# Performance work log

Hardware: AMD Instinct MI355X
Metric: run time of the kernel (lower is better)

Reference implementation:

```python
import jax, jax.numpy as jnp
import numpy as np

N_NODES = 100000
N_EDGES = 640000
F_IN = 128
HID = 128
N_CLS = 40


def _glorot(key, fan_in, fan_out):
    lim = float(np.sqrt(6.0 / (fan_in + fan_out)))
    return jax.random.uniform(key, (fan_in, fan_out), jnp.float32, -lim, lim)


def setup_inputs() -> dict:
    key = jax.random.key(0)
    ks = jax.random.split(key, 10)
    x = jax.random.normal(ks[0], (N_NODES, F_IN), jnp.float32)
    edge_index = jax.random.randint(ks[1], (2, N_EDGES), 0, N_NODES, jnp.int64 if jax.config.jax_enable_x64 else jnp.int32)
    W1 = _glorot(ks[2], F_IN, HID)
    W2 = _glorot(ks[3], HID, HID)
    W3 = _glorot(ks[4], HID, HID)
    W4 = _glorot(ks[5], HID, N_CLS)
    b1 = jnp.zeros((HID,), jnp.float32)
    b2 = jnp.zeros((HID,), jnp.float32)
    b3 = jnp.zeros((HID,), jnp.float32)
    b4 = jnp.zeros((N_CLS,), jnp.float32)
    return {"x": x, "edge_index": edge_index,
            "W1": W1, "b1": b1, "W2": W2, "b2": b2,
            "W3": W3, "b3": b3, "W4": W4, "b4": b4}


def _prep_edges(edge_index, n):
    # add self-loops, compute symmetric normalization deg^{-1/2}[src]*deg^{-1/2}[dst]
    loop = jnp.arange(n, dtype=edge_index.dtype)
    src = jnp.concatenate([edge_index[0], loop])
    dst = jnp.concatenate([edge_index[1], loop])
    deg = jax.ops.segment_sum(jnp.ones_like(dst, jnp.float32), dst, num_segments=n)
    dinv = jnp.where(deg > 0, jax.lax.rsqrt(deg), 0.0)
    norm = dinv[src] * dinv[dst]  # [E + n]
    return src, dst, norm


def _gcn_conv(x, W, b, src, dst, norm, n):
    h = x @ W                      # dense linear transform [n, out]
    msg = h[src] * norm[:, None]   # gather + scale over edges
    out = jax.ops.segment_sum(msg, dst, num_segments=n)  # scatter-add
    return out + b


def reference(x, edge_index, W1, b1, W2, b2, W3, b3, W4, b4):
    n = x.shape[0]
    src, dst, norm = _prep_edges(edge_index, n)
    h = jax.nn.relu(_gcn_conv(x, W1, b1, src, dst, norm, n))
    h = jax.nn.relu(_gcn_conv(h, W2, b2, src, dst, norm, n))
    h = jax.nn.relu(_gcn_conv(h, W3, b3, src, dst, norm, n))
    h = _gcn_conv(h, W4, b4, src, dst, norm, n)
    return jax.nn.log_softmax(h, axis=1)
```

## Files before the change

### kernel.cpp

```cpp
#include <hip/hip_runtime.h>
#include <math.h>

#define N_NODES 100000
#define N_EDGES 640000

typedef __bf16 bf16x8 __attribute__((ext_vector_type(8)));
typedef float f32x4 __attribute__((ext_vector_type(4)));

__device__ __forceinline__ unsigned short f2b(float x) {
  unsigned int u = __float_as_uint(x);
  u = (u + 0x7FFFu + ((u >> 16) & 1u)) >> 16;
  return (unsigned short)u;
}
__device__ __forceinline__ float blo(unsigned int v) { return __uint_as_float(v << 16); }
__device__ __forceinline__ float bhi(unsigned int v) { return __uint_as_float(v & 0xFFFF0000u); }


__global__ __launch_bounds__(256) void k_count(const int* __restrict__ dst, int* __restrict__ deg, int e) {
  int i = blockIdx.x * 256 + threadIdx.x;
  if (i < e) atomicAdd(&deg[dst[i]], 1);
}

__global__ __launch_bounds__(256) void k_alloc(const int* __restrict__ deg, int* __restrict__ row_ptr,
                                               int* __restrict__ fillpos, int* __restrict__ col,
                                               float* __restrict__ dinv, int* __restrict__ counter, int n) {
  __shared__ int sdata[256];
  __shared__ int sbase;
  int tid = threadIdx.x;
  int i = blockIdx.x * 256 + tid;
  int d = (i < n) ? deg[i] : 0;
  sdata[tid] = d;
  __syncthreads();
  for (int off = 1; off < 256; off <<= 1) {
    int v = (tid >= off) ? sdata[tid - off] : 0;
    __syncthreads();
    sdata[tid] += v;
    __syncthreads();
  }
  if (tid == 255) sbase = atomicAdd(counter, sdata[255]);
  __syncthreads();
  int base = sbase;
  if (i < n) {
    int rp = base + sdata[tid] - d;
    row_ptr[i] = rp;
    fillpos[i] = rp + 1;
    col[rp] = i;
    dinv[i] = rsqrtf((float)d);
  }
}

__global__ __launch_bounds__(256) void k_fill(const int* __restrict__ src, const int* __restrict__ dst,
                                              int* __restrict__ fillpos, int* __restrict__ col, int e) {
  int i = blockIdx.x * 256 + threadIdx.x;
  if (i < e) {
    int d = dst[i];
    int p = atomicAdd(&fillpos[d], 1);
    col[p] = src[i];
  }
}


__global__ __launch_bounds__(256) void k_prep0(const float* __restrict__ W1, const float* __restrict__ W2,
                                               const float* __restrict__ W3, const float* __restrict__ W4,
                                               unsigned short* __restrict__ Wt, unsigned short* __restrict__ Wt4,
                                               unsigned short* __restrict__ Ha, unsigned short* __restrict__ Hc,
                                               unsigned short* __restrict__ H4,
                                               int* __restrict__ deg, int* __restrict__ counter, int n) {
  int b = blockIdx.x;
  int tid = threadIdx.x;
  if (b < 391) {
    int i = b * 256 + tid;
    if (i < n) deg[i] = 1;
    if (i == 0) *counter = 0;
  } else if (b < 583) {
    int bb = b - 391;
    const float* W = (bb < 64) ? W1 : (bb < 128) ? W2 : W3;
    unsigned short* D = Wt + ((bb < 64) ? 0 : (bb < 128) ? 16384 : 32768);
    int idx = (bb & 63) * 256 + tid;
    int k = idx >> 7, nn = idx & 127;
    D[nn * 128 + k] = f2b(W[idx]);
  } else if (b < 607) {
    int idx = (b - 583) * 256 + tid;
    int nn = idx >> 7, k = idx & 127;
    Wt4[nn * 128 + k] = (nn < 40) ? f2b(W4[(size_t)k * 40 + nn]) : (unsigned short)0;
  } else if (b == 607) {
    if (tid < 128) Ha[(size_t)n * 128 + tid] = 0;
    else Hc[(size_t)n * 128 + (tid - 128)] = 0;
  } else {
    if (tid < 48) H4[(size_t)n * 40 + tid] = 0;
  }
}

#define SXP 136


__global__ __launch_bounds__(256) void k_gemm1(const float* __restrict__ X,
                                               const unsigned short* __restrict__ Wt,
                                               const float* __restrict__ dinv,
                                               unsigned short* __restrict__ H, int n) {
  __shared__ unsigned short sW[128 * SXP];
  int tid = threadIdx.x;
  int row0 = blockIdx.x * 64;
  {
    const uint4* Wt4 = (const uint4*)Wt;
#pragma unroll
    for (int i = 0; i < 8; ++i) {
      int f = tid + i * 256;
      *(uint4*)&sW[(f >> 4) * SXP + (f & 15) * 8] = Wt4[f];
    }
  }
  int wave = tid >> 6, lane = tid & 63;
  int m = lane & 15, q = lane >> 4;
  int grow = row0 + wave * 16 + m;
  if (grow >= n) grow = n - 1;
  const float4* X4 = (const float4*)X;
  uint4 a4[4];
#pragma unroll
  for (int kc = 0; kc < 4; ++kc) {
    float4 f0 = X4[(size_t)grow * 32 + kc * 8 + q * 2];
    float4 f1 = X4[(size_t)grow * 32 + kc * 8 + q * 2 + 1];
    a4[kc].x = (unsigned int)f2b(f0.x) | ((unsigned int)f2b(f0.y) << 16);
    a4[kc].y = (unsigned int)f2b(f0.z) | ((unsigned int)f2b(f0.w) << 16);
    a4[kc].z = (unsigned int)f2b(f1.x) | ((unsigned int)f2b(f1.y) << 16);
    a4[kc].w = (unsigned int)f2b(f1.z) | ((unsigned int)f2b(f1.w) << 16);
  }
  __syncthreads();
  f32x4 acc[8];
#pragma unroll
  for (int ct = 0; ct < 8; ++ct) acc[ct] = (f32x4){0.f, 0.f, 0.f, 0.f};
#pragma unroll
  for (int kc = 0; kc < 4; ++kc) {
    bf16x8 a = *(bf16x8*)&a4[kc];
#pragma unroll
    for (int ct = 0; ct < 8; ++ct) {
      bf16x8 b = *(const bf16x8*)&sW[(ct * 16 + m) * SXP + kc * 32 + q * 8];
      acc[ct] = __builtin_amdgcn_mfma_f32_16x16x32_bf16(a, b, acc[ct], 0, 0, 0);
    }
  }
#pragma unroll
  for (int r = 0; r < 4; ++r) {
    int row = row0 + wave * 16 + q * 4 + r;
    if (row < n) {
      float di = dinv[row];
#pragma unroll
      for (int ct = 0; ct < 8; ++ct)
        H[(size_t)row * 128 + ct * 16 + m] = f2b(acc[ct][r] * di);
    }
  }
}


template <int NCT>
__global__ __launch_bounds__(256) void k_fag(const unsigned short* __restrict__ Hin,
                                             const int* __restrict__ col,
                                             const int* __restrict__ row_ptr,
                                             const int* __restrict__ deg,
                                             const float* __restrict__ dinv,
                                             const float* __restrict__ bias,
                                             const unsigned short* __restrict__ Wt,
                                             unsigned short* __restrict__ Hout, int n) {
  __shared__ unsigned short sW[NCT * 16 * SXP];
  __shared__ unsigned short sX[64 * SXP];
  int tid = threadIdx.x;
  int row0 = blockIdx.x * 64;
  {
    const uint4* W4 = (const uint4*)Wt;
#pragma unroll
    for (int i = 0; i < NCT; ++i) {
      int f = tid + i * 256;
      *(uint4*)&sW[(f >> 4) * SXP + (f & 15) * 8] = W4[f];
    }
  }
  int ql = tid & 15;
  int qbase = tid & 48;
  const uint4* Hg = (const uint4*)Hin;
  float4 b0 = ((const float4*)bias)[ql * 2];
  float4 b1 = ((const float4*)bias)[ql * 2 + 1];
  int starts[4], cnts[4], mycs[4];
#pragma unroll
  for (int it = 0; it < 4; ++it) {
    int node = row0 + (tid >> 4) + (it << 4);
    int nc = (node < n) ? node : 0;
    starts[it] = row_ptr[nc];
    cnts[it] = deg[nc];
  }
#pragma unroll
  for (int it = 0; it < 4; ++it) {
    int c0 = (cnts[it] < 15) ? cnts[it] : 15;
    mycs[it] = (ql < c0) ? col[starts[it] + ql] : n;
  }
#pragma unroll 1
  for (int it = 0; it < 4; ++it) {
    int node = row0 + (tid >> 4) + (it << 4);
    if (node >= n) break;
    int cnt = cnts[it];
    int cnt0 = (cnt < 15) ? cnt : 15;
    int myc = mycs[it];
    float s0 = 0.f, s1 = 0.f, s2 = 0.f, s3 = 0.f, s4 = 0.f, s5 = 0.f, s6 = 0.f, s7 = 0.f;
    for (int base = 0; base < cnt0; base += 8) {
      uint4 v[8];
#pragma unroll
      for (int jj = 0; jj < 8; ++jj) {
        int idx = base + jj;
        idx = (idx > 15) ? 15 : idx;
        int c = __shfl(myc, qbase + idx, 64);
        v[jj] = Hg[(size_t)c * 16 + ql];
      }
#pragma unroll
      for (int jj = 0; jj < 8; ++jj) {
        s0 += blo(v[jj].x); s1 += bhi(v[jj].x);
        s2 += blo(v[jj].y); s3 += bhi(v[jj].y);
        s4 += blo(v[jj].z); s5 += bhi(v[jj].z);
        s6 += blo(v[jj].w); s7 += bhi(v[jj].w);
      }
    }
    for (int j = 15; j < cnt; ++j) {
      int c = col[starts[it] + j];
      uint4 v = Hg[(size_t)c * 16 + ql];
      s0 += blo(v.x); s1 += bhi(v.x);
      s2 += blo(v.y); s3 += bhi(v.y);
      s4 += blo(v.z); s5 += bhi(v.z);
      s6 += blo(v.w); s7 += bhi(v.w);
    }
    float di = dinv[node];
    float o0 = fmaf(s0, di, b0.x), o1 = fmaf(s1, di, b0.y);
    float o2 = fmaf(s2, di, b0.z), o3 = fmaf(s3, di, b0.w);
    float o4 = fmaf(s4, di, b1.x), o5 = fmaf(s5, di, b1.y);
    float o6 = fmaf(s6, di, b1.z), o7 = fmaf(s7, di, b1.w);
    o0 = o0 > 0.f ? o0 : 0.f; o1 = o1 > 0.f ? o1 : 0.f;
    o2 = o2 > 0.f ? o2 : 0.f; o3 = o3 > 0.f ? o3 : 0.f;
    o4 = o4 > 0.f ? o4 : 0.f; o5 = o5 > 0.f ? o5 : 0.f;
    o6 = o6 > 0.f ? o6 : 0.f; o7 = o7 > 0.f ? o7 : 0.f;
    uint4 w;
    w.x = (unsigned int)f2b(o0) | ((unsigned int)f2b(o1) << 16);
    w.y = (unsigned int)f2b(o2) | ((unsigned int)f2b(o3) << 16);
    w.z = (unsigned int)f2b(o4) | ((unsigned int)f2b(o5) << 16);
    w.w = (unsigned int)f2b(o6) | ((unsigned int)f2b(o7) << 16);
    *(uint4*)&sX[(node - row0) * SXP + ql * 8] = w;
  }
  __syncthreads();
  int wave = tid >> 6, lane = tid & 63;
  int m = lane & 15, q = lane >> 4;
  int grow = row0 + wave * 16 + m;
  if (grow >= n) grow = n - 1;
  int lrow = grow - row0;
  uint4 a4[4];
#pragma unroll
  for (int kc = 0; kc < 4; ++kc) a4[kc] = *(const uint4*)&sX[lrow * SXP + kc * 32 + q * 8];
  f32x4 acc[NCT];
#pragma unroll
  for (int ct = 0; ct < NCT; ++ct) acc[ct] = (f32x4){0.f, 0.f, 0.f, 0.f};
#pragma unroll
  for (int kc = 0; kc < 4; ++kc) {
    bf16x8 a = *(bf16x8*)&a4[kc];
#pragma unroll
    for (int ct = 0; ct < NCT; ++ct) {
      bf16x8 b = *(const bf16x8*)&sW[(ct * 16 + m) * SXP + kc * 32 + q * 8];
      acc[ct] = __builtin_amdgcn_mfma_f32_16x16x32_bf16(a, b, acc[ct], 0, 0, 0);
    }
  }
#pragma unroll
  for (int r = 0; r < 4; ++r) {
    int row = row0 + wave * 16 + q * 4 + r;
    if (row < n) {
      float di = dinv[row];
      if constexpr (NCT == 8) {
#pragma unroll
        for (int ct = 0; ct < 8; ++ct)
          Hout[(size_t)row * 128 + ct * 16 + m] = f2b(acc[ct][r] * di);
      } else {
#pragma unroll
        for (int ct = 0; ct < NCT; ++ct) {
          int c = ct * 16 + m;
          if (c < 40) Hout[(size_t)row * 40 + c] = f2b(acc[ct][r] * di);
        }
      }
    }
  }
}


__global__ __launch_bounds__(256) void k_agg40_lsm(const unsigned short* __restrict__ H, const int* __restrict__ col,
                                                   const int* __restrict__ row_ptr, const int* __restrict__ deg,
                                                   const float* __restrict__ dinv, const float* __restrict__ bias,
                                                   float* __restrict__ out, int n) {
  int node = blockIdx.x * 4 + (threadIdx.x >> 6);
  int lane = threadIdx.x & 63;
  if (node >= n) return;
  const unsigned int* H1 = (const unsigned int*)H;
  int start = row_ptr[node];
  int cnt = deg[node];
  int cnt0 = (cnt < 63) ? cnt : 63;
  int myc = (lane < cnt0) ? col[start + lane] : n;
  int slice = (lane >= 20) + (lane >= 40);
  int pr = lane - slice * 20;
  pr = (pr > 19) ? 19 : pr;
  int rounds = (cnt0 + 2) / 3;
  float ax = 0.f, ay = 0.f;
  for (int rb = 0; rb < rounds; rb += 4) {
    unsigned int v[4];
#pragma unroll
    for (int j = 0; j < 4; ++j) {
      int idx = (rb + j) * 3 + slice;
      idx = (idx > 63) ? 63 : idx;
      int c = __shfl(myc, idx, 64);
      v[j] = H1[(size_t)c * 20 + pr];
    }
#pragma unroll
    for (int j = 0; j < 4; ++j) { ax += blo(v[j]); ay += bhi(v[j]); }
  }
  if (lane < 20) {
    for (int j = 63; j < cnt; ++j) {
      int c = col[start + j];
      unsigned int v = H1[(size_t)c * 20 + pr];
      ax += blo(v);
      ay += bhi(v);
    }
  }
  float ax1 = __shfl(ax, lane + 20, 64), ay1 = __shfl(ay, lane + 20, 64);
  float ax2 = __shfl(ax, lane + 40, 64), ay2 = __shfl(ay, lane + 40, 64);
  float di = dinv[node];
  float2 b2 = ((const float2*)bias)[pr];
  float c0 = fmaf(ax + ax1 + ax2, di, b2.x);
  float c1 = fmaf(ay + ay1 + ay2, di, b2.y);
  float v = (lane < 20) ? fmaxf(c0, c1) : -INFINITY;
#pragma unroll
  for (int off = 32; off > 0; off >>= 1) v = fmaxf(v, __shfl_xor(v, off, 64));
  float e = (lane < 20) ? (__expf(c0 - v) + __expf(c1 - v)) : 0.f;
#pragma unroll
  for (int off = 32; off > 0; off >>= 1) e += __shfl_xor(e, off, 64);
  if (lane < 20) {
    float ls = v + __logf(e);
    ((float2*)out)[(size_t)node * 20 + lane] = make_float2(c0 - ls, c1 - ls);
  }
}


extern "C" void kernel_launch(void* const* d_in, const int* in_sizes, int n_in,
                              void* d_out, int out_size, void* d_ws, size_t ws_size,
                              hipStream_t stream) {
  const float* x  = (const float*)d_in[0];
  const int* edge = (const int*)d_in[1];
  const float* W1 = (const float*)d_in[2];
  const float* b1 = (const float*)d_in[3];
  const float* W2 = (const float*)d_in[4];
  const float* b2 = (const float*)d_in[5];
  const float* W3 = (const float*)d_in[6];
  const float* b3 = (const float*)d_in[7];
  const float* W4 = (const float*)d_in[8];
  const float* b4 = (const float*)d_in[9];
  float* out = (float*)d_out;

  const int n = N_NODES, E = N_EDGES;
  const int* srcp = edge;
  const int* dstp = edge + E;

  char* ws = (char*)d_ws;
  size_t off = 0;
  auto alloc = [&](size_t bytes) -> void* {
    void* p = ws + off;
    off = (off + bytes + 255) & ~(size_t)255;
    return p;
  };
  int*   deg     = (int*)alloc((size_t)n * 4);
  int*   row_ptr = (int*)alloc((size_t)n * 4);
  int*   fillpos = (int*)alloc((size_t)n * 4);
  float* dinv    = (float*)alloc((size_t)n * 4);
  int*   counter = (int*)alloc(256);
  int*   colx    = (int*)alloc((size_t)(E + n) * 4);
  unsigned short* Ha  = (unsigned short*)alloc((size_t)(n + 1) * 128 * 2);
  unsigned short* Hc  = (unsigned short*)alloc((size_t)(n + 1) * 128 * 2);
  unsigned short* H4  = (unsigned short*)alloc(((size_t)(n + 1) * 40 + 16) * 2);
  unsigned short* Wt  = (unsigned short*)alloc((size_t)3 * 128 * 128 * 2);
  unsigned short* Wt4 = (unsigned short*)alloc((size_t)48 * 128 * 2);
  (void)ws_size; (void)in_sizes; (void)n_in; (void)out_size;

  k_prep0<<<609, 256, 0, stream>>>(W1, W2, W3, W4, Wt, Wt4, Ha, Hc, H4, deg, counter, n);
  k_count<<<(E + 255) / 256, 256, 0, stream>>>(dstp, deg, E);
  k_alloc<<<(n + 255) / 256, 256, 0, stream>>>(deg, row_ptr, fillpos, colx, dinv, counter, n);
  k_fill <<<(E + 255) / 256, 256, 0, stream>>>(srcp, dstp, fillpos, colx, E);

  const int gg = (n + 63) / 64, ga = (n + 3) / 4;
  k_gemm1<<<gg, 256, 0, stream>>>(x, Wt, dinv, Ha, n);
  k_fag<8><<<gg, 256, 0, stream>>>(Ha, colx, row_ptr, deg, dinv, b1, Wt + 16384, Hc, n);
  k_fag<8><<<gg, 256, 0, stream>>>(Hc, colx, row_ptr, deg, dinv, b2, Wt + 32768, Ha, n);
  k_fag<3><<<gg, 256, 0, stream>>>(Ha, colx, row_ptr, deg, dinv, b3, Wt4, H4, n);
  k_agg40_lsm<<<ga, 256, 0, stream>>>(H4, colx, row_ptr, deg, dinv, b4, out, n);
}
```

Measured before the change: 331.8 us.

## Pre-swizzle weights into MFMA fragment order and load B directly from global

The weight matrices are now written at prep time in MFMA B-fragment order, so each lane reads its bf16x8 operand with one coalesced 16-byte global load. This removes the per-block staging of weights into LDS and the barrier in the GEMM and fused aggregate-GEMM kernels, cutting LDS use (which may raise occupancy) and per-block setup. In exchange, every wave re-reads the weights from L2/L1 instead of sharing one LDS copy, which relies on cache hits for the small weight matrices.

```diff
diff --git a/kernel.cpp b/kernel.cpp
--- a/kernel.cpp
+++ b/kernel.cpp
@@ -14,6 +14,12 @@
 }
 __device__ __forceinline__ float blo(unsigned int v) { return __uint_as_float(v << 16); }
 __device__ __forceinline__ float bhi(unsigned int v) { return __uint_as_float(v & 0xFFFF0000u); }
+
+__device__ __forceinline__ int fragidx(int nn, int k) {
+  int ct = nn >> 4, m = nn & 15;
+  int kc = k >> 5, q = (k >> 3) & 3, e = k & 7;
+  return (((ct * 4 + kc) * 4 + q) * 16 + m) * 8 + e;
+}
 
 
 __global__ __launch_bounds__(256) void k_count(const int* __restrict__ dst, int* __restrict__ deg, int e) {
@@ -78,11 +84,11 @@
     unsigned short* D = Wt + ((bb < 64) ? 0 : (bb < 128) ? 16384 : 32768);
     int idx = (bb & 63) * 256 + tid;
     int k = idx >> 7, nn = idx & 127;
-    D[nn * 128 + k] = f2b(W[idx]);
+    D[fragidx(nn, k)] = f2b(W[idx]);
   } else if (b < 607) {
     int idx = (b - 583) * 256 + tid;
     int nn = idx >> 7, k = idx & 127;
-    Wt4[nn * 128 + k] = (nn < 40) ? f2b(W4[(size_t)k * 40 + nn]) : (unsigned short)0;
+    Wt4[fragidx(nn, k)] = (nn < 40) ? f2b(W4[(size_t)k * 40 + nn]) : (unsigned short)0;
   } else if (b == 607) {
     if (tid < 128) Ha[(size_t)n * 128 + tid] = 0;
     else Hc[(size_t)n * 128 + (tid - 128)] = 0;
@@ -98,17 +104,8 @@
                                                const unsigned short* __restrict__ Wt,
                                                const float* __restrict__ dinv,
                                                unsigned short* __restrict__ H, int n) {
-  __shared__ unsigned short sW[128 * SXP];
   int tid = threadIdx.x;
   int row0 = blockIdx.x * 64;
-  {
-    const uint4* Wt4 = (const uint4*)Wt;
-#pragma unroll
-    for (int i = 0; i < 8; ++i) {
-      int f = tid + i * 256;
-      *(uint4*)&sW[(f >> 4) * SXP + (f & 15) * 8] = Wt4[f];
-    }
-  }
   int wave = tid >> 6, lane = tid & 63;
   int m = lane & 15, q = lane >> 4;
   int grow = row0 + wave * 16 + m;
@@ -124,7 +121,7 @@
     a4[kc].z = (unsigned int)f2b(f1.x) | ((unsigned int)f2b(f1.y) << 16);
     a4[kc].w = (unsigned int)f2b(f1.z) | ((unsigned int)f2b(f1.w) << 16);
   }
-  __syncthreads();
+  const bf16x8* Wf = (const bf16x8*)Wt;
   f32x4 acc[8];
 #pragma unroll
   for (int ct = 0; ct < 8; ++ct) acc[ct] = (f32x4){0.f, 0.f, 0.f, 0.f};
@@ -133,7 +130,7 @@
     bf16x8 a = *(bf16x8*)&a4[kc];
 #pragma unroll
     for (int ct = 0; ct < 8; ++ct) {
-      bf16x8 b = *(const bf16x8*)&sW[(ct * 16 + m) * SXP + kc * 32 + q * 8];
+      bf16x8 b = Wf[(ct * 4 + kc) * 64 + lane];
       acc[ct] = __builtin_amdgcn_mfma_f32_16x16x32_bf16(a, b, acc[ct], 0, 0, 0);
     }
   }
@@ -159,18 +156,9 @@
                                              const float* __restrict__ bias,
                                              const unsigned short* __restrict__ Wt,
                                              unsigned short* __restrict__ Hout, int n) {
-  __shared__ unsigned short sW[NCT * 16 * SXP];
   __shared__ unsigned short sX[64 * SXP];
   int tid = threadIdx.x;
   int row0 = blockIdx.x * 64;
-  {
-    const uint4* W4 = (const uint4*)Wt;
-#pragma unroll
-    for (int i = 0; i < NCT; ++i) {
-      int f = tid + i * 256;
-      *(uint4*)&sW[(f >> 4) * SXP + (f & 15) * 8] = W4[f];
-    }
-  }
   int ql = tid & 15;
   int qbase = tid & 48;
   const uint4* Hg = (const uint4*)Hin;
@@ -247,6 +235,7 @@
   uint4 a4[4];
 #pragma unroll
   for (int kc = 0; kc < 4; ++kc) a4[kc] = *(const uint4*)&sX[lrow * SXP + kc * 32 + q * 8];
+  const bf16x8* Wf = (const bf16x8*)Wt;
   f32x4 acc[NCT];
 #pragma unroll
   for (int ct = 0; ct < NCT; ++ct) acc[ct] = (f32x4){0.f, 0.f, 0.f, 0.f};
@@ -255,7 +244,7 @@
     bf16x8 a = *(bf16x8*)&a4[kc];
 #pragma unroll
     for (int ct = 0; ct < NCT; ++ct) {
-      bf16x8 b = *(const bf16x8*)&sW[(ct * 16 + m) * SXP + kc * 32 + q * 8];
+      bf16x8 b = Wf[(ct * 4 + kc) * 64 + lane];
       acc[ct] = __builtin_amdgcn_mfma_f32_16x16x32_bf16(a, b, acc[ct], 0, 0, 0);
     }
   }
```

Result: slower. 340.6 us (+2.6%).

## Pad last-layer features to 64 and aggregate with 8 lanes per node using 16-byte loads

Applied to the files above, without the earlier changes.

The last-layer hidden buffer is padded from 40 to 64 bf16 columns so each row is 128 bytes, and the final GEMM writes all 4 column tiles without masking. The aggregation plus log-softmax kernel now gives each node 8 lanes, each gathering a 16-byte chunk per neighbor, instead of 64 lanes doing 4-byte loads split three ways. This cuts instruction count and improves coalescing of the gather. In exchange it adds padding bandwidth and wastes 3 of 8 lanes, and the extra MFMA tile adds a little compute.

```diff
diff --git a/kernel.cpp b/kernel.cpp
--- a/kernel.cpp
+++ b/kernel.cpp
@@ -79,15 +79,15 @@
     int idx = (bb & 63) * 256 + tid;
     int k = idx >> 7, nn = idx & 127;
     D[nn * 128 + k] = f2b(W[idx]);
-  } else if (b < 607) {
+  } else if (b < 615) {
     int idx = (b - 583) * 256 + tid;
     int nn = idx >> 7, k = idx & 127;
     Wt4[nn * 128 + k] = (nn < 40) ? f2b(W4[(size_t)k * 40 + nn]) : (unsigned short)0;
-  } else if (b == 607) {
+  } else if (b == 615) {
     if (tid < 128) Ha[(size_t)n * 128 + tid] = 0;
     else Hc[(size_t)n * 128 + (tid - 128)] = 0;
   } else {
-    if (tid < 48) H4[(size_t)n * 40 + tid] = 0;
+    if (tid < 64) H4[(size_t)n * 64 + tid] = 0;
   }
 }
 
@@ -270,10 +270,8 @@
           Hout[(size_t)row * 128 + ct * 16 + m] = f2b(acc[ct][r] * di);
       } else {
 #pragma unroll
-        for (int ct = 0; ct < NCT; ++ct) {
-          int c = ct * 16 + m;
-          if (c < 40) Hout[(size_t)row * 40 + c] = f2b(acc[ct][r] * di);
-        }
+        for (int ct = 0; ct < NCT; ++ct)
+          Hout[(size_t)row * 64 + ct * 16 + m] = f2b(acc[ct][r] * di);
       }
     }
   }
@@ -284,54 +282,58 @@
                                                    const int* __restrict__ row_ptr, const int* __restrict__ deg,
                                                    const float* __restrict__ dinv, const float* __restrict__ bias,
                                                    float* __restrict__ out, int n) {
-  int node = blockIdx.x * 4 + (threadIdx.x >> 6);
-  int lane = threadIdx.x & 63;
+  int node = blockIdx.x * 32 + (threadIdx.x >> 3);
+  int ol = threadIdx.x & 7;
+  int obase = threadIdx.x & 56;
   if (node >= n) return;
-  const unsigned int* H1 = (const unsigned int*)H;
+  const uint4* Hg = (const uint4*)H;
   int start = row_ptr[node];
   int cnt = deg[node];
-  int cnt0 = (cnt < 63) ? cnt : 63;
-  int myc = (lane < cnt0) ? col[start + lane] : n;
-  int slice = (lane >= 20) + (lane >= 40);
-  int pr = lane - slice * 20;
-  pr = (pr > 19) ? 19 : pr;
-  int rounds = (cnt0 + 2) / 3;
-  float ax = 0.f, ay = 0.f;
-  for (int rb = 0; rb < rounds; rb += 4) {
-    unsigned int v[4];
-#pragma unroll
-    for (int j = 0; j < 4; ++j) {
-      int idx = (rb + j) * 3 + slice;
-      idx = (idx > 63) ? 63 : idx;
-      int c = __shfl(myc, idx, 64);
-      v[j] = H1[(size_t)c * 20 + pr];
-    }
-#pragma unroll
-    for (int j = 0; j < 4; ++j) { ax += blo(v[j]); ay += bhi(v[j]); }
-  }
-  if (lane < 20) {
-    for (int j = 63; j < cnt; ++j) {
-      int c = col[start + j];
-      unsigned int v = H1[(size_t)c * 20 + pr];
-      ax += blo(v);
-      ay += bhi(v);
-    }
-  }
-  float ax1 = __shfl(ax, lane + 20, 64), ay1 = __shfl(ay, lane + 20, 64);
-  float ax2 = __shfl(ax, lane + 40, 64), ay2 = __shfl(ay, lane + 40, 64);
+  float a0 = 0.f, a1 = 0.f, a2 = 0.f, a3 = 0.f, a4 = 0.f, a5 = 0.f, a6 = 0.f, a7 = 0.f;
+  for (int rb = 0; rb < cnt; rb += 8) {
+    int myc = (rb + ol < cnt) ? col[start + rb + ol] : n;
+    uint4 v[8];
+#pragma unroll
+    for (int jj = 0; jj < 8; ++jj) {
+      int c = __shfl(myc, obase + jj, 64);
+      v[jj] = Hg[(size_t)c * 8 + ol];
+    }
+#pragma unroll
+    for (int jj = 0; jj < 8; ++jj) {
+      a0 += blo(v[jj].x); a1 += bhi(v[jj].x);
+      a2 += blo(v[jj].y); a3 += bhi(v[jj].y);
+      a4 += blo(v[jj].z); a5 += bhi(v[jj].z);
+      a6 += blo(v[jj].w); a7 += bhi(v[jj].w);
+    }
+  }
   float di = dinv[node];
-  float2 b2 = ((const float2*)bias)[pr];
-  float c0 = fmaf(ax + ax1 + ax2, di, b2.x);
-  float c1 = fmaf(ay + ay1 + ay2, di, b2.y);
-  float v = (lane < 20) ? fmaxf(c0, c1) : -INFINITY;
-#pragma unroll
-  for (int off = 32; off > 0; off >>= 1) v = fmaxf(v, __shfl_xor(v, off, 64));
-  float e = (lane < 20) ? (__expf(c0 - v) + __expf(c1 - v)) : 0.f;
-#pragma unroll
-  for (int off = 32; off > 0; off >>= 1) e += __shfl_xor(e, off, 64);
-  if (lane < 20) {
-    float ls = v + __logf(e);
-    ((float2*)out)[(size_t)node * 20 + lane] = make_float2(c0 - ls, c1 - ls);
+  bool valid = (ol < 5);
+  float c0, c1, c2, c3, c4, c5, c6, c7;
+  if (valid) {
+    float4 bb0 = ((const float4*)bias)[ol * 2];
+    float4 bb1 = ((const float4*)bias)[ol * 2 + 1];
+    c0 = fmaf(a0, di, bb0.x); c1 = fmaf(a1, di, bb0.y);
+    c2 = fmaf(a2, di, bb0.z); c3 = fmaf(a3, di, bb0.w);
+    c4 = fmaf(a4, di, bb1.x); c5 = fmaf(a5, di, bb1.y);
+    c6 = fmaf(a6, di, bb1.z); c7 = fmaf(a7, di, bb1.w);
+  } else {
+    c0 = c1 = c2 = c3 = c4 = c5 = c6 = c7 = -INFINITY;
+  }
+  float m = fmaxf(fmaxf(fmaxf(c0, c1), fmaxf(c2, c3)), fmaxf(fmaxf(c4, c5), fmaxf(c6, c7)));
+  m = fmaxf(m, __shfl_xor(m, 1, 8));
+  m = fmaxf(m, __shfl_xor(m, 2, 8));
+  m = fmaxf(m, __shfl_xor(m, 4, 8));
+  float e = valid ? (__expf(c0 - m) + __expf(c1 - m) + __expf(c2 - m) + __expf(c3 - m) +
+                     __expf(c4 - m) + __expf(c5 - m) + __expf(c6 - m) + __expf(c7 - m)) : 0.f;
+  e += __shfl_xor(e, 1, 8);
+  e += __shfl_xor(e, 2, 8);
+  e += __shfl_xor(e, 4, 8);
+  if (valid) {
+    float ls = m + __logf(e);
+    float4 o0 = {c0 - ls, c1 - ls, c2 - ls, c3 - ls};
+    float4 o1 = {c4 - ls, c5 - ls, c6 - ls, c7 - ls};
+    *(float4*)&out[(size_t)node * 40 + ol * 8] = o0;
+    *(float4*)&out[(size_t)node * 40 + ol * 8 + 4] = o1;
   }
 }
 
@@ -370,20 +372,20 @@
   int*   colx    = (int*)alloc((size_t)(E + n) * 4);
   unsigned short* Ha  = (unsigned short*)alloc((size_t)(n + 1) * 128 * 2);
   unsigned short* Hc  = (unsigned short*)alloc((size_t)(n + 1) * 128 * 2);
-  unsigned short* H4  = (unsigned short*)alloc(((size_t)(n + 1) * 40 + 16) * 2);
+  unsigned short* H4  = (unsigned short*)alloc((size_t)(n + 1) * 64 * 2);
   unsigned short* Wt  = (unsigned short*)alloc((size_t)3 * 128 * 128 * 2);
-  unsigned short* Wt4 = (unsigned short*)alloc((size_t)48 * 128 * 2);
+  unsigned short* Wt4 = (unsigned short*)alloc((size_t)64 * 128 * 2);
   (void)ws_size; (void)in_sizes; (void)n_in; (void)out_size;
 
-  k_prep0<<<609, 256, 0, stream>>>(W1, W2, W3, W4, Wt, Wt4, Ha, Hc, H4, deg, counter, n);
+  k_prep0<<<617, 256, 0, stream>>>(W1, W2, W3, W4, Wt, Wt4, Ha, Hc, H4, deg, counter, n);
   k_count<<<(E + 255) / 256, 256, 0, stream>>>(dstp, deg, E);
   k_alloc<<<(n + 255) / 256, 256, 0, stream>>>(deg, row_ptr, fillpos, colx, dinv, counter, n);
   k_fill <<<(E + 255) / 256, 256, 0, stream>>>(srcp, dstp, fillpos, colx, E);
 
-  const int gg = (n + 63) / 64, ga = (n + 3) / 4;
+  const int gg = (n + 63) / 64, ga = (n + 31) / 32;
   k_gemm1<<<gg, 256, 0, stream>>>(x, Wt, dinv, Ha, n);
   k_fag<8><<<gg, 256, 0, stream>>>(Ha, colx, row_ptr, deg, dinv, b1, Wt + 16384, Hc, n);
   k_fag<8><<<gg, 256, 0, stream>>>(Hc, colx, row_ptr, deg, dinv, b2, Wt + 32768, Ha, n);
-  k_fag<3><<<gg, 256, 0, stream>>>(Ha, colx, row_ptr, deg, dinv, b3, Wt4, H4, n);
+  k_fag<4><<<gg, 256, 0, stream>>>(Ha, colx, row_ptr, deg, dinv, b3, Wt4, H4, n);
   k_agg40_lsm<<<ga, 256, 0, stream>>>(H4, colx, row_ptr, deg, dinv, b4, out, n);
 }
```

Result: faster. 318.5 us (-4.0%).
